# Performance work log

Hardware: AMD Instinct MI355X
Metric: run time of the kernel (lower is better)

## Reference

```python
import jax, jax.numpy as jnp
import numpy as np

N_NODES = 50000
IN_F, HID_F, OUT_F = 256, 128, 40
N_EDGES = 800000


def _uniform(key, shape, scale):
    return jax.random.uniform(key, shape, dtype=jnp.float32, minval=-scale, maxval=scale)


def setup_inputs() -> dict:
    key = jax.random.key(0)
    ks = jax.random.split(key, 20)
    x = jax.random.normal(ks[0], (N_NODES, IN_F), dtype=jnp.float32)
    edge_index = jax.random.randint(ks[1], (2, N_EDGES), 0, N_NODES, dtype=jnp.int64)
    s0, sa0 = 1.0 / np.sqrt(HID_F), 1.0  # std_att = 1/sqrt(1)
    s1, sa1 = 1.0 / np.sqrt(OUT_F), 1.0
    sv = 1.0 / np.sqrt(3.0)
    return {
        "x": x, "edge_index": edge_index,
        "Wl0": _uniform(ks[2], (IN_F, HID_F), s0),
        "Wh0": _uniform(ks[3], (IN_F, HID_F), s0),
        "Wm0": _uniform(ks[4], (IN_F, HID_F), s0),
        "al0": _uniform(ks[5], (HID_F, 1), sa0),
        "ah0": _uniform(ks[6], (HID_F, 1), sa0),
        "am0": _uniform(ks[7], (HID_F, 1), sa0),
        "att0": _uniform(ks[8], (3, 3), sv),
        "Wl1": _uniform(ks[9], (HID_F, OUT_F), s1),
        "Wh1": _uniform(ks[10], (HID_F, OUT_F), s1),
        "Wm1": _uniform(ks[11], (HID_F, OUT_F), s1),
        "al1": _uniform(ks[12], (OUT_F, 1), sa1),
        "ah1": _uniform(ks[13], (OUT_F, 1), sa1),
        "am1": _uniform(ks[14], (OUT_F, 1), sa1),
        "att1": _uniform(ks[15], (3, 3), sv),
    }


def _acm_layer(x, row, col, d_inv, Wl, Wh, Wm, al, ah, am, att):
    n = x.shape[0]
    hl, hh, hm = x @ Wl, x @ Wh, x @ Wm
    # adj_low @ M  with adj_low = D^{-1}(I + A): gather sources, scatter-add to rows
    def low(M):
        return d_inv[:, None] * (M + jax.ops.segment_sum(M[col], row, num_segments=n))
    out_low = jax.nn.relu(low(hl))
    out_high = jax.nn.relu(hh - low(hh))  # adj_high = I - adj_low
    out_mlp = jax.nn.relu(hm)
    T = 3.0
    sig = jax.nn.sigmoid(jnp.concatenate([out_low @ al, out_high @ ah, out_mlp @ am], axis=1))  # [n,3]
    a = jax.nn.softmax((sig @ att) / T, axis=1)
    return 3.0 * (a[:, 0:1] * out_low + a[:, 1:2] * out_high + a[:, 2:3] * out_mlp)


def reference(x, edge_index, Wl0, Wh0, Wm0, al0, ah0, am0, att0,
              Wl1, Wh1, Wm1, al1, ah1, am1, att1):
    n = x.shape[0]
    row, col = edge_index[0], edge_index[1]
    deg = jax.ops.segment_sum(jnp.ones_like(row, dtype=jnp.float32), row, num_segments=n)
    rowsum = 1.0 + deg  # rowsum of I + A (duplicates counted, as in scipy)
    d_inv = jnp.where(rowsum > 0, 1.0 / rowsum, 0.0)
    h = _acm_layer(x, row, col, d_inv, Wl0, Wh0, Wm0, al0, ah0, am0, att0)
    out = _acm_layer(h, row, col, d_inv, Wl1, Wh1, Wm1, al1, ah1, am1, att1)
    return out
```

## Files before the change

### kernel.cpp

```cpp
#include <hip/hip_runtime.h>
#include <math.h>

#define N_NODES 50000
#define N_EDGES 800000
#define IN_F    256
#define HID_F   128
#define OUT_F   40
#define W0N     (3*HID_F)
#define W1N     (3*OUT_F)
#define NB      ((N_NODES + 255) / 256)

#define SEG     128
#define EPB     (N_EDGES / SEG)
#define NWORD   (N_NODES / 2)
#define WB      ((NWORD + 255) / 256)

#define XB   ((N_NODES * IN_F) / (256 * 16))
#define P0B  ((IN_F * W0N) / 256)
#define P1B  ((HID_F * W1N) / 256)
#define HPB0 (SEG)
#define HPB1 (SEG + XB)
#define HPB2 (SEG + XB + P0B)
#define HPREPB (SEG + XB + P0B + P1B)

typedef __attribute__((ext_vector_type(8))) unsigned short ushort8;
typedef __attribute__((ext_vector_type(4))) unsigned short ushort4v;
typedef __attribute__((ext_vector_type(8))) __bf16 bf16x8;
typedef __attribute__((ext_vector_type(4))) float f32x4;
typedef __attribute__((ext_vector_type(2))) float f32x2;

static __device__ __forceinline__ float sigmoidf_(float x) {
    return 1.0f / (1.0f + expf(-x));
}

static __device__ __forceinline__ unsigned short f2bf(float f) {
    unsigned u = __float_as_uint(f);
    u += 0x7FFFu + ((u >> 16) & 1u);
    return (unsigned short)(u >> 16);
}

static __device__ __forceinline__ float bflo(unsigned u) { return __uint_as_float(u << 16); }
static __device__ __forceinline__ float bfhi(unsigned u) { return __uint_as_float(u & 0xffff0000u); }
static __device__ __forceinline__ int rfl(int v) { return __builtin_amdgcn_readfirstlane(v); }


__global__ __launch_bounds__(256) void k_hp(
        const int* __restrict__ ei, unsigned* __restrict__ segHist,
        unsigned short* __restrict__ rank, unsigned* __restrict__ rc,
        const float* __restrict__ x, unsigned short* __restrict__ xb,
        const float* __restrict__ Wl0, const float* __restrict__ Wh0,
        const float* __restrict__ Wm0, unsigned short* __restrict__ W0t,
        const float* __restrict__ Wl1, const float* __restrict__ Wh1,
        const float* __restrict__ Wm1, unsigned short* __restrict__ W1t) {
    __shared__ unsigned hist[NWORD];
    int b = blockIdx.x, t = threadIdx.x;
    if (b < SEG) {
        int seg = b;
        for (int i = t; i < NWORD; i += 256) hist[i] = 0;
        __syncthreads();
        int base = seg * EPB;
        for (int k2 = t; k2 < EPB / 2; k2 += 256) {
            int e = base + k2 * 2;
            int2 rv = *(const int2*)(ei + e);
            int2 cv = *(const int2*)(ei + N_EDGES + e);
            unsigned o0 = atomicAdd(&hist[rv.x >> 1], (rv.x & 1) ? 0x10000u : 1u);
            unsigned l0 = (rv.x & 1) ? (o0 >> 16) : (o0 & 0xffffu);
            unsigned o1 = atomicAdd(&hist[rv.y >> 1], (rv.y & 1) ? 0x10000u : 1u);
            unsigned l1 = (rv.y & 1) ? (o1 >> 16) : (o1 & 0xffffu);
            ushort2 rk;
            rk.x = (unsigned short)l0; rk.y = (unsigned short)l1;
            *(ushort2*)(rank + e) = rk;
            uint2 rcv;
            rcv.x = ((unsigned)rv.x << 16) | (unsigned)cv.x;
            rcv.y = ((unsigned)rv.y << 16) | (unsigned)cv.y;
            *(uint2*)(rc + e) = rcv;
        }
        __syncthreads();
        unsigned* dst = segHist + (size_t)seg * NWORD;
        for (int i = t; i < NWORD; i += 256) dst[i] = hist[i];
    } else if (b < HPB1) {
        size_t idx = (size_t)(b - HPB0) * 4096 + t * 16;
        float4 f0 = *(const float4*)(x + idx);
        float4 f1 = *(const float4*)(x + idx + 4);
        float4 f2 = *(const float4*)(x + idx + 8);
        float4 f3 = *(const float4*)(x + idx + 12);
        ushort8 u0, u1;
        u0[0]=f2bf(f0.x); u0[1]=f2bf(f0.y); u0[2]=f2bf(f0.z); u0[3]=f2bf(f0.w);
        u0[4]=f2bf(f1.x); u0[5]=f2bf(f1.y); u0[6]=f2bf(f1.z); u0[7]=f2bf(f1.w);
        u1[0]=f2bf(f2.x); u1[1]=f2bf(f2.y); u1[2]=f2bf(f2.z); u1[3]=f2bf(f2.w);
        u1[4]=f2bf(f3.x); u1[5]=f2bf(f3.y); u1[6]=f2bf(f3.z); u1[7]=f2bf(f3.w);
        *(ushort8*)(xb + idx)     = u0;
        *(ushort8*)(xb + idx + 8) = u1;
    } else if (b < HPB2) {
        int i = (b - HPB1) * 256 + t;
        int n = i / IN_F, k = i % IN_F;
        float v;
        if (n < HID_F)            v = Wl0[k * HID_F + n];
        else if (n < 2 * HID_F)   v = Wh0[k * HID_F + (n - HID_F)];
        else                      v = Wm0[k * HID_F + (n - 2 * HID_F)];
        W0t[i] = f2bf(v);
    } else {
        int i = (b - HPB2) * 256 + t;
        int n = i / HID_F, kp = i % HID_F;
        int k = ((kp >> 6) << 6) + ((kp & 3) << 4) + ((kp >> 2) & 15);
        float v;
        if (n < OUT_F)            v = Wl1[k * OUT_F + n];
        else if (n < 2 * OUT_F)   v = Wh1[k * OUT_F + (n - OUT_F)];
        else                      v = Wm1[k * OUT_F + (n - 2 * OUT_F)];
        W1t[i] = f2bf(v);
    }
}


__global__ __launch_bounds__(256) void k_scanseg(
        unsigned* __restrict__ segHist, int* __restrict__ rowPtr,
        float* __restrict__ dinv, int* __restrict__ blkTot) {
    __shared__ int s[256];
    int t = threadIdx.x;
    int w = blockIdx.x * 256 + t;
    int cum0 = 0, cum1 = 0;
    if (w < NWORD) {
        for (int sg = 0; sg < SEG; ++sg) {
            size_t idx = (size_t)sg * NWORD + w;
            unsigned h = segHist[idx];
            segHist[idx] = ((unsigned)cum1 << 16) | (unsigned)cum0;
            cum0 += (int)(h & 0xffffu);
            cum1 += (int)(h >> 16);
        }
    }
    int deg0 = cum0, deg1 = cum1;
    int pair = deg0 + deg1;
    s[t] = pair; __syncthreads();
    for (int d = 1; d < 256; d <<= 1) {
        int x = (t >= d) ? s[t - d] : 0;
        __syncthreads();
        s[t] += x;
        __syncthreads();
    }
    int basep = s[t] - pair;
    if (w < NWORD) {
        rowPtr[2 * w]     = basep;
        rowPtr[2 * w + 1] = basep + deg0;
        dinv[2 * w]     = 1.0f / (1.0f + (float)deg0);
        dinv[2 * w + 1] = 1.0f / (1.0f + (float)deg1);
    }
    if (t == 255) blkTot[blockIdx.x] = s[255];
}


__global__ void k_scan3(const int* __restrict__ blkTot, int* __restrict__ rowPtr) {
    int t = threadIdx.x;
    int b = blockIdx.x;
    int m = b >> 1;
    int lane = t & 63;
    int v = 0;
    if (lane < m) v = blkTot[lane];
    if (lane + 64 < m) v += blkTot[lane + 64];
#pragma unroll
    for (int d = 1; d < 64; d <<= 1) v += __shfl_xor(v, d);
    int gid = b * 256 + t;
    if (gid < N_NODES) rowPtr[gid] += v;
    if (gid == 0) rowPtr[N_NODES] = N_EDGES;
}


#define BKP 40

template<int EPI>
__global__ __launch_bounds__(256) void k_gemm_fill(
        const unsigned short* __restrict__ A, const unsigned short* __restrict__ Bt,
        unsigned short* __restrict__ C0, int ld0,
        unsigned short* __restrict__ C1, int ld1, int nsplit,
        unsigned char* __restrict__ Cq,
        unsigned short* __restrict__ Hs, unsigned char* __restrict__ Hq,
        unsigned short* __restrict__ HmP,
        int M, int N, int K, int nxt,
        const unsigned* __restrict__ rc, const unsigned short* __restrict__ rank,
        const int* __restrict__ rowPtr, const unsigned short* __restrict__ segOff,
        unsigned short* __restrict__ colIdx) {
    __shared__ unsigned short As[128 * BKP];
    __shared__ unsigned short Bs[128 * BKP];
    int tid  = threadIdx.x;

    if ((int)blockIdx.x >= nxt) {
        int fid = (blockIdx.x - nxt) * gridDim.y + blockIdx.y;
        int e = fid * 256 + tid;
        if (e < N_EDGES) {
            unsigned x = rc[e];
            int r = (int)(x >> 16);
            int seg = e / EPB;
            int pos = rowPtr[r] + (int)segOff[(size_t)seg * N_NODES + r] + (int)rank[e];
            colIdx[pos] = (unsigned short)(x & 0xffffu);
        }
        return;
    }

    int lane = tid & 63, wid = tid >> 6;
    int wr = wid >> 1, wc = wid & 1;
    int bm = blockIdx.y * 128, bn = blockIdx.x * 128;

    int srow = tid >> 1;
    int scol = (tid & 1) * 16;

    int garow = min(bm + srow, M - 1);
    int gbrow = min(bn + srow, N - 1);

    f32x4 acc[4][4];
#pragma unroll
    for (int m = 0; m < 4; ++m)
#pragma unroll
        for (int n = 0; n < 4; ++n)
            acc[m][n] = (f32x4)(0.0f);

    int kg = (lane >> 4) * 8;
    int rA = wr * 64 + (lane & 15);
    int rB = wc * 64 + (lane & 15);

    const unsigned short* srcA = A + (size_t)garow * K + scol;
    const unsigned short* srcB = Bt + (size_t)gbrow * K + scol;
    ushort8 ra0 = *(const ushort8*)(srcA);
    ushort8 ra1 = *(const ushort8*)(srcA + 8);
    ushort8 rb0 = *(const ushort8*)(srcB);
    ushort8 rb1 = *(const ushort8*)(srcB + 8);

    for (int k0 = 0; k0 < K; k0 += 32) {
        *(ushort8*)&As[srow * BKP + scol]     = ra0;
        *(ushort8*)&As[srow * BKP + scol + 8] = ra1;
        *(ushort8*)&Bs[srow * BKP + scol]     = rb0;
        *(ushort8*)&Bs[srow * BKP + scol + 8] = rb1;
        __syncthreads();
        if (k0 + 32 < K) {
            ra0 = *(const ushort8*)(srcA + k0 + 32);
            ra1 = *(const ushort8*)(srcA + k0 + 40);
            rb0 = *(const ushort8*)(srcB + k0 + 32);
            rb1 = *(const ushort8*)(srcB + k0 + 40);
        }

        bf16x8 a[4], b[4];
#pragma unroll
        for (int m = 0; m < 4; ++m)
            a[m] = __builtin_bit_cast(bf16x8, *(const ushort8*)&As[(rA + m * 16) * BKP + kg]);
#pragma unroll
        for (int n = 0; n < 4; ++n)
            b[n] = __builtin_bit_cast(bf16x8, *(const ushort8*)&Bs[(rB + n * 16) * BKP + kg]);
#pragma unroll
        for (int m = 0; m < 4; ++m)
#pragma unroll
            for (int n = 0; n < 4; ++n)
                acc[m][n] = __builtin_amdgcn_mfma_f32_16x16x32_bf16(a[m], b[n], acc[m][n], 0, 0, 0);
        __syncthreads();
    }

    int col  = lane & 15;
    int rsub = (lane >> 4) * 4;

    if (EPI == 0) {
#pragma unroll
        for (int m = 0; m < 4; ++m) {
            int gm0 = bm + wr * 64 + m * 16 + rsub;
#pragma unroll
            for (int n = 0; n < 4; ++n) {
                int gn = bn + wc * 64 + n * 16 + col;
                if (gn >= N) continue;
#pragma unroll
                for (int j = 0; j < 4; ++j) {
                    int gm = gm0 + j;
                    if (gm >= M) continue;
                    float v = acc[m][n][j];
                    unsigned short b = f2bf(v);
                    if (gn < nsplit) {
                        C0[(size_t)gm * ld0 + gn] = b;
                        int pk = __builtin_amdgcn_cvt_pk_fp8_f32(v, v, 0, false);
                        Cq[(size_t)gm * nsplit + gn] = (unsigned char)(pk & 0xff);
                    } else {
                        C1[(size_t)gm * ld1 + (gn - nsplit)] = b;
                    }
                }
            }
        }
    } else {
#pragma unroll
        for (int m = 0; m < 4; ++m) {
            int gm0 = bm + wr * 64 + m * 16 + rsub;
#pragma unroll
            for (int j = 0; j < 4; ++j) {
                int gm = gm0 + j;
                if (gm >= M) continue;
                float v0 = acc[m][0][j], v1 = acc[m][1][j];
                float v2 = acc[m][2][j], v3 = acc[m][3][j];
                ushort4v o;
                o[0] = f2bf(v0); o[1] = f2bf(v1); o[2] = f2bf(v2); o[3] = f2bf(v3);
                if (bn < 256) {
                    int pos = bn + wc * 64 + col * 4;
                    *(ushort4v*)&Hs[(size_t)gm * 256 + pos] = o;
                    int pk = 0;
                    pk = __builtin_amdgcn_cvt_pk_fp8_f32(v0, v1, pk, false);
                    pk = __builtin_amdgcn_cvt_pk_fp8_f32(v2, v3, pk, true);
                    *(unsigned*)&Hq[(size_t)gm * 256 + pos] = (unsigned)pk;
                } else {
                    int pos = wc * 64 + col * 4;
                    *(ushort4v*)&HmP[(size_t)gm * 128 + pos] = o;
                }
            }
        }
    }
}


__global__ __launch_bounds__(256) void k_layer0(
        const unsigned short* __restrict__ Hs, const unsigned char* __restrict__ Hq,
        const unsigned short* __restrict__ HmP,
        const int* __restrict__ rowPtr, const unsigned short* __restrict__ colIdx,
        const float* __restrict__ dinv,
        const float* __restrict__ al, const float* __restrict__ ah,
        const float* __restrict__ am, const float* __restrict__ att,
        unsigned short* __restrict__ hout) {
    int lane = threadIdx.x & 63;
    int i = blockIdx.x * 4 + (threadIdx.x >> 6);

    int p0 = rfl(rowPtr[i]);
    int p1 = rfl(rowPtr[i + 1]);
    int deg = p1 - p0;
    f32x2 A01 = {0.f, 0.f}, A23 = {0.f, 0.f};
    int off4 = lane * 4;

    auto gath = [&](int js) -> unsigned {
        return *(const unsigned*)(Hq + ((size_t)(unsigned)js << 8) + off4);
    };
    auto addw = [&](unsigned w) {
        A01 += __builtin_amdgcn_cvt_pk_f32_fp8((int)w, false);
        A23 += __builtin_amdgcn_cvt_pk_f32_fp8((int)w, true);
    };

    for (int c = 0; c < deg; c += 64) {
        int rem = deg - c; if (rem > 64) rem = 64;
        int mycol = (int)colIdx[p0 + c + (lane < rem ? lane : 0)];
        int q = 0;
        for (; q + 7 < rem; q += 8) {
            int j0 = rfl(__shfl(mycol, q + 0));
            int j1 = rfl(__shfl(mycol, q + 1));
            int j2 = rfl(__shfl(mycol, q + 2));
            int j3 = rfl(__shfl(mycol, q + 3));
            int j4 = rfl(__shfl(mycol, q + 4));
            int j5 = rfl(__shfl(mycol, q + 5));
            int j6 = rfl(__shfl(mycol, q + 6));
            int j7 = rfl(__shfl(mycol, q + 7));
            unsigned w0 = gath(j0), w1 = gath(j1), w2 = gath(j2), w3 = gath(j3);
            unsigned w4 = gath(j4), w5 = gath(j5), w6 = gath(j6), w7 = gath(j7);
            addw(w0); addw(w1); addw(w2); addw(w3);
            addw(w4); addw(w5); addw(w6); addw(w7);
        }
        for (; q < rem; ++q) {
            int j = rfl(__shfl(mycol, q));
            addw(gath(j));
        }
    }
    float a0 = A01.x, a1 = A01.y, a2 = A23.x, a3 = A23.y;

    uint2 sv = *(const uint2*)(Hs + (size_t)i * 256 + off4);
    float s0 = bflo(sv.x), s1 = bfhi(sv.x), s2 = bflo(sv.y), s3 = bfhi(sv.y);
    float di = dinv[i];
    float l0 = di * (s0 + a0), l1 = di * (s1 + a1);
    float l2 = di * (s2 + a2), l3 = di * (s3 + a3);

    float ol0 = fmaxf(l0, 0.f), ol1 = fmaxf(l1, 0.f);
    float ol2 = fmaxf(l2, 0.f), ol3 = fmaxf(l3, 0.f);
    float oh0 = fmaxf(s0 - l0, 0.f), oh1 = fmaxf(s1 - l1, 0.f);
    float oh2 = fmaxf(s2 - l2, 0.f), oh3 = fmaxf(s3 - l3, 0.f);

    int c0 = ((lane >> 4) << 6) + (lane & 15);

    float om0 = 0.f, om1 = 0.f, om2 = 0.f, om3 = 0.f;
    float prA, prM = 0.f;
    if (lane < 32) {
        uint2 hv = *(const uint2*)(HmP + (size_t)i * 128 + off4);
        om0 = fmaxf(bflo(hv.x), 0.f); om1 = fmaxf(bfhi(hv.x), 0.f);
        om2 = fmaxf(bflo(hv.y), 0.f); om3 = fmaxf(bfhi(hv.y), 0.f);
        prA = ol0 * al[c0] + ol1 * al[c0 + 16] + ol2 * al[c0 + 32] + ol3 * al[c0 + 48];
        prM = om0 * am[c0] + om1 * am[c0 + 16] + om2 * am[c0 + 32] + om3 * am[c0 + 48];
    } else {
        int ch = c0 - 128;
        prA = oh0 * ah[ch] + oh1 * ah[ch + 16] + oh2 * ah[ch + 32] + oh3 * ah[ch + 48];
    }

#pragma unroll
    for (int d = 1; d < 32; d <<= 1) prA += __shfl_xor(prA, d);
#pragma unroll
    for (int d = 1; d < 32; d <<= 1) prM += __shfl_xor(prM, d);
    float g0 = __shfl(prA, 0);
    float g1 = __shfl(prA, 32);
    float g2 = __shfl(prM, 0);

    float sg0 = sigmoidf_(g0), sg1 = sigmoidf_(g1), sg2 = sigmoidf_(g2);
    const float inv3 = (1.0f / 3.0f);
    float e0 = (sg0 * att[0] + sg1 * att[3] + sg2 * att[6]) * inv3;
    float e1 = (sg0 * att[1] + sg1 * att[4] + sg2 * att[7]) * inv3;
    float e2 = (sg0 * att[2] + sg1 * att[5] + sg2 * att[8]) * inv3;
    float mx = fmaxf(e0, fmaxf(e1, e2));
    float x0 = expf(e0 - mx), x1 = expf(e1 - mx), x2 = expf(e2 - mx);
    float inv = 1.0f / (x0 + x1 + x2);
    float c0f = 3.0f * inv * x0, c1f = 3.0f * inv * x1, c2f = 3.0f * inv * x2;

    int src = lane | 32;
    float th0 = __shfl(oh0, src), th1 = __shfl(oh1, src);
    float th2 = __shfl(oh2, src), th3 = __shfl(oh3, src);

    if (lane < 32) {
        ushort4v o;
        o[0] = f2bf(c0f * ol0 + c1f * th0 + c2f * om0);
        o[1] = f2bf(c0f * ol1 + c1f * th1 + c2f * om1);
        o[2] = f2bf(c0f * ol2 + c1f * th2 + c2f * om2);
        o[3] = f2bf(c0f * ol3 + c1f * th3 + c2f * om3);
        *(ushort4v*)&hout[(size_t)i * 128 + off4] = o;
    }
}


__global__ __launch_bounds__(256) void k_layer1(
        const unsigned short* __restrict__ H1g, const unsigned char* __restrict__ H1q,
        const unsigned short* __restrict__ H1m,
        const int* __restrict__ rowPtr, const unsigned short* __restrict__ colIdx,
        const float* __restrict__ dinv,
        const float* __restrict__ al, const float* __restrict__ ah,
        const float* __restrict__ am, const float* __restrict__ att,
        float* __restrict__ out) {
    int lane = threadIdx.x & 63;
    int i = blockIdx.x * 4 + (threadIdx.x >> 6);

    int p0 = rfl(rowPtr[i]);
    int p1 = rfl(rowPtr[i + 1]);
    int deg = p1 - p0;
    f32x2 A01 = {0.f, 0.f}, A23 = {0.f, 0.f};
    bool active = lane < 20;
    int off4 = lane * 4;
    int offc = active ? off4 : 0;

    auto gath = [&](int js) -> unsigned {
        return *(const unsigned*)(H1q + (size_t)((unsigned)js * 80u) + offc);
    };
    auto addw = [&](unsigned w) {
        A01 += __builtin_amdgcn_cvt_pk_f32_fp8((int)w, false);
        A23 += __builtin_amdgcn_cvt_pk_f32_fp8((int)w, true);
    };

    for (int c = 0; c < deg; c += 64) {
        int rem = deg - c; if (rem > 64) rem = 64;
        int mycol = (int)colIdx[p0 + c + (lane < rem ? lane : 0)];
        int q = 0;
        for (; q + 7 < rem; q += 8) {
            int j0 = rfl(__shfl(mycol, q + 0));
            int j1 = rfl(__shfl(mycol, q + 1));
            int j2 = rfl(__shfl(mycol, q + 2));
            int j3 = rfl(__shfl(mycol, q + 3));
            int j4 = rfl(__shfl(mycol, q + 4));
            int j5 = rfl(__shfl(mycol, q + 5));
            int j6 = rfl(__shfl(mycol, q + 6));
            int j7 = rfl(__shfl(mycol, q + 7));
            unsigned w0 = gath(j0), w1 = gath(j1), w2 = gath(j2), w3 = gath(j3);
            unsigned w4 = gath(j4), w5 = gath(j5), w6 = gath(j6), w7 = gath(j7);
            addw(w0); addw(w1); addw(w2); addw(w3);
            addw(w4); addw(w5); addw(w6); addw(w7);
        }
        for (; q < rem; ++q) {
            int j = rfl(__shfl(mycol, q));
            addw(gath(j));
        }
    }
    float a0 = A01.x, a1 = A01.y, a2 = A23.x, a3 = A23.y;

    float s0 = 0.f, s1 = 0.f, s2 = 0.f, s3 = 0.f;
    if (active) {
        uint2 sv = *(const uint2*)(H1g + (size_t)i * 80 + off4);
        s0 = bflo(sv.x); s1 = bfhi(sv.x); s2 = bflo(sv.y); s3 = bfhi(sv.y);
    }
    float di = dinv[i];
    float l0 = di * (s0 + a0), l1 = di * (s1 + a1);
    float l2 = di * (s2 + a2), l3 = di * (s3 + a3);

    float ol0 = fmaxf(l0, 0.f), ol1 = fmaxf(l1, 0.f);
    float ol2 = fmaxf(l2, 0.f), ol3 = fmaxf(l3, 0.f);
    float oh0 = fmaxf(s0 - l0, 0.f), oh1 = fmaxf(s1 - l1, 0.f);
    float oh2 = fmaxf(s2 - l2, 0.f), oh3 = fmaxf(s3 - l3, 0.f);

    float om0 = 0.f, om1 = 0.f, om2 = 0.f, om3 = 0.f;
    float r0 = 0.f, r1 = 0.f, r2 = 0.f;
    if (lane < 10) {
        uint2 hv = *(const uint2*)(H1m + (size_t)i * 40 + off4);
        om0 = fmaxf(bflo(hv.x), 0.f); om1 = fmaxf(bfhi(hv.x), 0.f);
        om2 = fmaxf(bflo(hv.y), 0.f); om3 = fmaxf(bfhi(hv.y), 0.f);
        float4 alv = *(const float4*)(al + off4);
        float4 amv = *(const float4*)(am + off4);
        r0 = ol0 * alv.x + ol1 * alv.y + ol2 * alv.z + ol3 * alv.w;
        r2 = om0 * amv.x + om1 * amv.y + om2 * amv.z + om3 * amv.w;
    } else if (lane < 20) {
        float4 ahv = *(const float4*)(ah + (off4 - 40));
        r1 = oh0 * ahv.x + oh1 * ahv.y + oh2 * ahv.z + oh3 * ahv.w;
    }

#pragma unroll
    for (int d = 1; d < 64; d <<= 1) r0 += __shfl_xor(r0, d);
#pragma unroll
    for (int d = 1; d < 64; d <<= 1) r1 += __shfl_xor(r1, d);
#pragma unroll
    for (int d = 1; d < 64; d <<= 1) r2 += __shfl_xor(r2, d);

    float sg0 = sigmoidf_(r0), sg1 = sigmoidf_(r1), sg2 = sigmoidf_(r2);
    const float inv3 = (1.0f / 3.0f);
    float e0 = (sg0 * att[0] + sg1 * att[3] + sg2 * att[6]) * inv3;
    float e1 = (sg0 * att[1] + sg1 * att[4] + sg2 * att[7]) * inv3;
    float e2 = (sg0 * att[2] + sg1 * att[5] + sg2 * att[8]) * inv3;
    float mx = fmaxf(e0, fmaxf(e1, e2));
    float x0 = expf(e0 - mx), x1 = expf(e1 - mx), x2 = expf(e2 - mx);
    float inv = 1.0f / (x0 + x1 + x2);
    float c0 = 3.0f * inv * x0, c1 = 3.0f * inv * x1, c2 = 3.0f * inv * x2;

    int src = (lane + 10) & 63;
    float th0 = __shfl(oh0, src), th1 = __shfl(oh1, src);
    float th2 = __shfl(oh2, src), th3 = __shfl(oh3, src);

    if (lane < 10) {
        float4 o;
        o.x = c0 * ol0 + c1 * th0 + c2 * om0;
        o.y = c0 * ol1 + c1 * th1 + c2 * om1;
        o.z = c0 * ol2 + c1 * th2 + c2 * om2;
        o.w = c0 * ol3 + c1 * th3 + c2 * om3;
        *(float4*)&out[(size_t)i * 40 + off4] = o;
    }
}


extern "C" void kernel_launch(void* const* d_in, const int* in_sizes, int n_in,
                              void* d_out, int out_size, void* d_ws, size_t ws_size,
                              hipStream_t stream) {
    const float* x    = (const float*)d_in[0];
    const int*   ei   = (const int*)d_in[1];
    const float* Wl0  = (const float*)d_in[2];
    const float* Wh0  = (const float*)d_in[3];
    const float* Wm0  = (const float*)d_in[4];
    const float* al0  = (const float*)d_in[5];
    const float* ah0  = (const float*)d_in[6];
    const float* am0  = (const float*)d_in[7];
    const float* att0 = (const float*)d_in[8];
    const float* Wl1  = (const float*)d_in[9];
    const float* Wh1  = (const float*)d_in[10];
    const float* Wm1  = (const float*)d_in[11];
    const float* al1  = (const float*)d_in[12];
    const float* ah1  = (const float*)d_in[13];
    const float* am1  = (const float*)d_in[14];
    const float* att1 = (const float*)d_in[15];
    float* out = (float*)d_out;

    char* ws = (char*)d_ws;
    size_t off = 0;
    auto alloc = [&](size_t bytes) -> char* {
        char* p = ws + off;
        off += (bytes + 255) & ~(size_t)255;
        return p;
    };
    int*      rowPtr  = (int*)     alloc((size_t)(N_NODES + 1) * 4);
    int*      blkTot  = (int*)     alloc(256 * 4);
    unsigned* segHist = (unsigned*)alloc((size_t)SEG * NWORD * 4);
    unsigned short* rank   = (unsigned short*)alloc((size_t)N_EDGES * 2);
    unsigned*       rc     = (unsigned*)      alloc((size_t)N_EDGES * 4);
    unsigned short* colIdx = (unsigned short*)alloc((size_t)N_EDGES * 2 + 256);
    float* dinv   = (float*)alloc((size_t)N_NODES * 4);
    unsigned short* W0t  = (unsigned short*)alloc((size_t)W0N * IN_F * 2);
    unsigned short* W1t  = (unsigned short*)alloc((size_t)W1N * HID_F * 2);
    unsigned short* xb   = (unsigned short*)alloc((size_t)N_NODES * IN_F * 2);
    unsigned short* Hs   = (unsigned short*)alloc((size_t)N_NODES * 256 * 2);
    unsigned char*  Hq   = (unsigned char*) alloc((size_t)N_NODES * 256);
    unsigned short* HmP  = (unsigned short*)alloc((size_t)N_NODES * 128 * 2);
    unsigned short* H1g  = (unsigned short*)alloc((size_t)N_NODES * 80 * 2);
    unsigned char*  H1q  = (unsigned char*) alloc((size_t)N_NODES * 80 + 256);
    unsigned short* H1m  = (unsigned short*)alloc((size_t)N_NODES * 40 * 2);
    unsigned short* hbuf = (unsigned short*)alloc((size_t)N_NODES * HID_F * 2);

    k_hp<<<HPREPB, 256, 0, stream>>>(ei, segHist, rank, rc,
                                     x, xb, Wl0, Wh0, Wm0, W0t,
                                     Wl1, Wh1, Wm1, W1t);
    k_scanseg<<<WB, 256, 0, stream>>>(segHist, rowPtr, dinv, blkTot);
    k_scan3<<<NB, 256, 0, stream>>>(blkTot, rowPtr);
    {
        dim3 grid(3 + 8, (N_NODES + 127) / 128);
        k_gemm_fill<1><<<grid, 256, 0, stream>>>(xb, W0t,
                                                 nullptr, 0, nullptr, 0, 0, nullptr,
                                                 Hs, Hq, HmP,
                                                 N_NODES, W0N, IN_F, 3,
                                                 rc, rank, rowPtr,
                                                 (const unsigned short*)segHist, colIdx);
    }
    k_layer0<<<N_NODES / 4, 256, 0, stream>>>(Hs, Hq, HmP, rowPtr, colIdx, dinv,
                                              al0, ah0, am0, att0, hbuf);
    {
        dim3 grid(1, (N_NODES + 127) / 128);
        k_gemm_fill<0><<<grid, 256, 0, stream>>>(hbuf, W1t,
                                                 H1g, 80, H1m, 40, 80, H1q,
                                                 nullptr, nullptr, nullptr,
                                                 N_NODES, W1N, HID_F, 1,
                                                 nullptr, nullptr, nullptr, nullptr, nullptr);
    }
    k_layer1<<<N_NODES / 4, 256, 0, stream>>>(H1g, H1q, H1m, rowPtr, colIdx, dinv,
                                              al1, ah1, am1, att1, out);
}
```

Before: 184.7 us.

## Split layer-0 gather into feature-chunked kernel with chunk-major fp8 layout

The fp8 feature table is stored chunk-major, in 8 column chunks of 32 bytes per node, so each gather kernel block touches only a 1.6MB slice that can stay cache-resident. A new gather kernel has each block handle one chunk for 16 nodes. Each 8-lane group fetches a different neighbour, and the partial sums are reduced across groups with shuffles. The aggregated sums go to a bf16 buffer that a separate epilogue kernel reads. This trades an extra kernel launch and an extra write and read of a 25MB intermediate, plus repeated colIdx reads per chunk, for better cache locality in the random gathers.

```diff
diff --git a/kernel.cpp b/kernel.cpp
--- a/kernel.cpp
+++ b/kernel.cpp
@@ -14,6 +14,8 @@
 #define EPB     (N_EDGES / SEG)
 #define NWORD   (N_NODES / 2)
 #define WB      ((NWORD + 255) / 256)
+
+#define CS      ((size_t)N_NODES * 32)
 
 #define XB   ((N_NODES * IN_F) / (256 * 16))
 #define P0B  ((IN_F * W0N) / 256)
@@ -147,7 +149,6 @@
     if (t == 255) blkTot[blockIdx.x] = s[255];
 }
 
-
 __global__ void k_scan3(const int* __restrict__ blkTot, int* __restrict__ rowPtr) {
     int t = threadIdx.x;
     int b = blockIdx.x;
@@ -172,7 +173,7 @@
         unsigned short* __restrict__ C0, int ld0,
         unsigned short* __restrict__ C1, int ld1, int nsplit,
         unsigned char* __restrict__ Cq,
-        unsigned short* __restrict__ Hs, unsigned char* __restrict__ Hq,
+        unsigned short* __restrict__ Hs, unsigned char* __restrict__ Hq2,
         unsigned short* __restrict__ HmP,
         int M, int N, int K, int nxt,
         const unsigned* __restrict__ rc, const unsigned short* __restrict__ rank,
@@ -296,7 +297,8 @@
                     int pk = 0;
                     pk = __builtin_amdgcn_cvt_pk_fp8_f32(v0, v1, pk, false);
                     pk = __builtin_amdgcn_cvt_pk_fp8_f32(v2, v3, pk, true);
-                    *(unsigned*)&Hq[(size_t)gm * 256 + pos] = (unsigned)pk;
+                    *(unsigned*)&Hq2[(size_t)(pos >> 5) * CS + (size_t)gm * 32 + (pos & 31)]
+                        = (unsigned)pk;
                 } else {
                     int pos = wc * 64 + col * 4;
                     *(ushort4v*)&HmP[(size_t)gm * 128 + pos] = o;
@@ -307,55 +309,87 @@
 }
 
 
-__global__ __launch_bounds__(256) void k_layer0(
-        const unsigned short* __restrict__ Hs, const unsigned char* __restrict__ Hq,
-        const unsigned short* __restrict__ HmP,
+__global__ __launch_bounds__(256) void k_gather(
+        const unsigned char* __restrict__ Hq2,
         const int* __restrict__ rowPtr, const unsigned short* __restrict__ colIdx,
+        unsigned short* __restrict__ agg) {
+    int lane = threadIdx.x & 63;
+    int wid  = threadIdx.x >> 6;
+    int chunk = blockIdx.x & 7;
+    int tile  = blockIdx.x >> 3;
+    int g = lane >> 3, s = lane & 7;
+    const unsigned char* base = Hq2 + (size_t)chunk * CS + s * 4;
+
+    for (int n = 0; n < 4; ++n) {
+        int i = tile * 16 + wid * 4 + n;
+        int p0 = rfl(rowPtr[i]);
+        int p1 = rfl(rowPtr[i + 1]);
+        int deg = p1 - p0;
+
+        f32x2 A01 = {0.f, 0.f}, A23 = {0.f, 0.f};
+
+        for (int c = 0; c < deg; c += 64) {
+            int rem = deg - c; if (rem > 64) rem = 64;
+            int mycol = (int)colIdx[p0 + c + (lane < rem ? lane : 0)];
+            int nfull = rem >> 3;
+            int q = 0;
+            for (; q + 1 < nfull; q += 2) {
+                int jA = __shfl(mycol, q * 8 + g);
+                int jB = __shfl(mycol, q * 8 + 8 + g);
+                unsigned wA = *(const unsigned*)(base + (unsigned)jA * 32u);
+                unsigned wB = *(const unsigned*)(base + (unsigned)jB * 32u);
+                A01 += __builtin_amdgcn_cvt_pk_f32_fp8((int)wA, false);
+                A23 += __builtin_amdgcn_cvt_pk_f32_fp8((int)wA, true);
+                A01 += __builtin_amdgcn_cvt_pk_f32_fp8((int)wB, false);
+                A23 += __builtin_amdgcn_cvt_pk_f32_fp8((int)wB, true);
+            }
+            for (; q < nfull; ++q) {
+                int j = __shfl(mycol, q * 8 + g);
+                unsigned w = *(const unsigned*)(base + (unsigned)j * 32u);
+                A01 += __builtin_amdgcn_cvt_pk_f32_fp8((int)w, false);
+                A23 += __builtin_amdgcn_cvt_pk_f32_fp8((int)w, true);
+            }
+            int done = nfull * 8;
+            if (done < rem) {
+                int j = __shfl(mycol, done + g);
+                unsigned w = *(const unsigned*)(base + (unsigned)j * 32u);
+                if (done + g < rem) {
+                    A01 += __builtin_amdgcn_cvt_pk_f32_fp8((int)w, false);
+                    A23 += __builtin_amdgcn_cvt_pk_f32_fp8((int)w, true);
+                }
+            }
+        }
+
+#pragma unroll
+        for (int d = 8; d < 64; d <<= 1) {
+            A01.x += __shfl_xor(A01.x, d);
+            A01.y += __shfl_xor(A01.y, d);
+            A23.x += __shfl_xor(A23.x, d);
+            A23.y += __shfl_xor(A23.y, d);
+        }
+        if (g == 0) {
+            ushort4v o;
+            o[0] = f2bf(A01.x); o[1] = f2bf(A01.y);
+            o[2] = f2bf(A23.x); o[3] = f2bf(A23.y);
+            *(ushort4v*)&agg[(size_t)i * 256 + chunk * 32 + s * 4] = o;
+        }
+    }
+}
+
+
+__global__ __launch_bounds__(256) void k_epi0(
+        const unsigned short* __restrict__ agg,
+        const unsigned short* __restrict__ Hs, const unsigned short* __restrict__ HmP,
         const float* __restrict__ dinv,
         const float* __restrict__ al, const float* __restrict__ ah,
         const float* __restrict__ am, const float* __restrict__ att,
         unsigned short* __restrict__ hout) {
     int lane = threadIdx.x & 63;
     int i = blockIdx.x * 4 + (threadIdx.x >> 6);
-
-    int p0 = rfl(rowPtr[i]);
-    int p1 = rfl(rowPtr[i + 1]);
-    int deg = p1 - p0;
-    f32x2 A01 = {0.f, 0.f}, A23 = {0.f, 0.f};
     int off4 = lane * 4;
 
-    auto gath = [&](int js) -> unsigned {
-        return *(const unsigned*)(Hq + ((size_t)(unsigned)js << 8) + off4);
-    };
-    auto addw = [&](unsigned w) {
-        A01 += __builtin_amdgcn_cvt_pk_f32_fp8((int)w, false);
-        A23 += __builtin_amdgcn_cvt_pk_f32_fp8((int)w, true);
-    };
-
-    for (int c = 0; c < deg; c += 64) {
-        int rem = deg - c; if (rem > 64) rem = 64;
-        int mycol = (int)colIdx[p0 + c + (lane < rem ? lane : 0)];
-        int q = 0;
-        for (; q + 7 < rem; q += 8) {
-            int j0 = rfl(__shfl(mycol, q + 0));
-            int j1 = rfl(__shfl(mycol, q + 1));
-            int j2 = rfl(__shfl(mycol, q + 2));
-            int j3 = rfl(__shfl(mycol, q + 3));
-            int j4 = rfl(__shfl(mycol, q + 4));
-            int j5 = rfl(__shfl(mycol, q + 5));
-            int j6 = rfl(__shfl(mycol, q + 6));
-            int j7 = rfl(__shfl(mycol, q + 7));
-            unsigned w0 = gath(j0), w1 = gath(j1), w2 = gath(j2), w3 = gath(j3);
-            unsigned w4 = gath(j4), w5 = gath(j5), w6 = gath(j6), w7 = gath(j7);
-            addw(w0); addw(w1); addw(w2); addw(w3);
-            addw(w4); addw(w5); addw(w6); addw(w7);
-        }
-        for (; q < rem; ++q) {
-            int j = rfl(__shfl(mycol, q));
-            addw(gath(j));
-        }
-    }
-    float a0 = A01.x, a1 = A01.y, a2 = A23.x, a3 = A23.y;
+    uint2 av = *(const uint2*)(agg + (size_t)i * 256 + off4);
+    float a0 = bflo(av.x), a1 = bfhi(av.x), a2 = bflo(av.y), a3 = bfhi(av.y);
 
     uint2 sv = *(const uint2*)(Hs + (size_t)i * 256 + off4);
     float s0 = bflo(sv.x), s1 = bfhi(sv.x), s2 = bflo(sv.y), s3 = bfhi(sv.y);
@@ -568,8 +602,9 @@
     unsigned short* W1t  = (unsigned short*)alloc((size_t)W1N * HID_F * 2);
     unsigned short* xb   = (unsigned short*)alloc((size_t)N_NODES * IN_F * 2);
     unsigned short* Hs   = (unsigned short*)alloc((size_t)N_NODES * 256 * 2);
-    unsigned char*  Hq   = (unsigned char*) alloc((size_t)N_NODES * 256);
+    unsigned char*  Hq2  = (unsigned char*) alloc((size_t)N_NODES * 256 + 256);
     unsigned short* HmP  = (unsigned short*)alloc((size_t)N_NODES * 128 * 2);
+    unsigned short* agg  = (unsigned short*)alloc((size_t)N_NODES * 256 * 2);
     unsigned short* H1g  = (unsigned short*)alloc((size_t)N_NODES * 80 * 2);
     unsigned char*  H1q  = (unsigned char*) alloc((size_t)N_NODES * 80 + 256);
     unsigned short* H1m  = (unsigned short*)alloc((size_t)N_NODES * 40 * 2);
@@ -584,13 +619,14 @@
         dim3 grid(3 + 8, (N_NODES + 127) / 128);
         k_gemm_fill<1><<<grid, 256, 0, stream>>>(xb, W0t,
                                                  nullptr, 0, nullptr, 0, 0, nullptr,
-                                                 Hs, Hq, HmP,
+                                                 Hs, Hq2, HmP,
                                                  N_NODES, W0N, IN_F, 3,
                                                  rc, rank, rowPtr,
                                                  (const unsigned short*)segHist, colIdx);
     }
-    k_layer0<<<N_NODES / 4, 256, 0, stream>>>(Hs, Hq, HmP, rowPtr, colIdx, dinv,
-                                              al0, ah0, am0, att0, hbuf);
+    k_gather<<<(N_NODES / 16) * 8, 256, 0, stream>>>(Hq2, rowPtr, colIdx, agg);
+    k_epi0<<<N_NODES / 4, 256, 0, stream>>>(agg, Hs, HmP, dinv,
+                                            al0, ah0, am0, att0, hbuf);
     {
         dim3 grid(1, (N_NODES + 127) / 128);
         k_gemm_fill<0><<<grid, 256, 0, stream>>>(hbuf, W1t,
```

Result: slower. 236.2 us (+27.9%).
